# Kernel tuning notes

Hardware: AMD Instinct MI355X
Metric: run time of the kernel (lower is better)

## Reference

```python
import jax, jax.numpy as jnp
import numpy as np

N = 4096          # num_nodes
E = 65536         # num edges (avg degree 16)
WALK_LENGTH = 16
OUT_DIM = 8


def setup_inputs() -> dict:
    key = jax.random.key(0)
    k1, k2 = jax.random.split(key, 2)
    edge_index = jax.random.randint(k1, (2, E), 0, N, dtype=jnp.int64)
    # nn.Linear(walk_length, out_dim): weight [out_dim, walk_length], bias [out_dim]
    linear_w = (jax.random.normal(k2, (OUT_DIM, WALK_LENGTH), jnp.float32)
                / np.float32(np.sqrt(WALK_LENGTH)))
    linear_b = jnp.zeros((OUT_DIM,), jnp.float32)
    return {"edge_index": edge_index, "num_nodes": N,
            "linear_w": linear_w, "linear_b": linear_b}


def reference(edge_index, num_nodes, linear_w, linear_b):
    row, col = edge_index[0], edge_index[1]
    # out-degree via scatter_add, clamped to >= 1
    deg = jnp.zeros((num_nodes,), jnp.float32).at[row].add(1.0)
    deg = jnp.maximum(deg, 1.0)
    rw_values = 1.0 / deg[row]                              # [E]
    # random-walk transition matrix P[row, col] = 1/deg[row]
    # (.at[].add sums duplicate edges, matching coalesce())
    P = jnp.zeros((num_nodes, num_nodes), jnp.float32).at[row, col].add(rw_values)
    Pt = P.T

    def step(cur, _):
        cur = Pt @ cur                                      # [N, N]
        return cur, jnp.diagonal(cur)                       # k-step return probs

    cur0 = jnp.eye(num_nodes, dtype=jnp.float32)
    _, diags = jax.lax.scan(step, cur0, None, length=WALK_LENGTH)
    rw_diag = diags.T                                       # [N, walk_length]
    return rw_diag @ linear_w.T + linear_b                  # [N, out_dim]
```

## Files before the change

### kernel.cpp

```cpp
#include <hip/hip_runtime.h>
#include <hip/hip_fp16.h>
#include <hip/hip_fp8.h>

#define NNODES 4096
#define LWALK 16
#define ODIM 8

#define FP8_SCALE 256.0f
#define FP8_INV   0.00390625f
#define FP8_INV2  1.52587890625e-05f

typedef unsigned int uint4n __attribute__((ext_vector_type(4)));
typedef unsigned int uint2n __attribute__((ext_vector_type(2)));
typedef float float2n __attribute__((ext_vector_type(2)));

__device__ __forceinline__ void dec8f(unsigned int lo, unsigned int hi, float* f) {
#if __has_builtin(__builtin_amdgcn_cvt_pk_f32_fp8)
    float2n p;
    p = __builtin_amdgcn_cvt_pk_f32_fp8((int)lo, false); f[0] = p.x; f[1] = p.y;
    p = __builtin_amdgcn_cvt_pk_f32_fp8((int)lo, true);  f[2] = p.x; f[3] = p.y;
    p = __builtin_amdgcn_cvt_pk_f32_fp8((int)hi, false); f[4] = p.x; f[5] = p.y;
    p = __builtin_amdgcn_cvt_pk_f32_fp8((int)hi, true);  f[6] = p.x; f[7] = p.y;
#else
    unsigned int w[2] = {lo, hi};
    const unsigned char* b = (const unsigned char*)w;
#pragma unroll
    for (int i = 0; i < 8; ++i) {
        __hip_fp8_e4m3 t; t.__x = b[i]; f[i] = (float)t;
    }
#endif
}

__device__ __forceinline__ void enc8f(const float* a, unsigned int* lo,
                                      unsigned int* hi) {
#if __has_builtin(__builtin_amdgcn_cvt_pk_fp8_f32)
    int l = 0, h = 0;
    l = __builtin_amdgcn_cvt_pk_fp8_f32(a[0], a[1], l, false);
    l = __builtin_amdgcn_cvt_pk_fp8_f32(a[2], a[3], l, true);
    h = __builtin_amdgcn_cvt_pk_fp8_f32(a[4], a[5], h, false);
    h = __builtin_amdgcn_cvt_pk_fp8_f32(a[6], a[7], h, true);
    *lo = (unsigned int)l; *hi = (unsigned int)h;
#else
    unsigned char b[8];
#pragma unroll
    for (int i = 0; i < 8; ++i)
        b[i] = __hip_cvt_float_to_fp8(a[i], __HIP_SATFINITE, __HIP_E4M3);
    unsigned int w[2];
    __builtin_memcpy(w, b, 8);
    *lo = w[0]; *hi = w[1];
#endif
}

__device__ __forceinline__ void dec16f(uint4n w, float* f) {
    dec8f(w.x, w.y, f);
    dec8f(w.z, w.w, f + 8);
}

__device__ __forceinline__ uint4n enc16f(const float* a) {
    uint4n o;
    unsigned int lo, hi;
    enc8f(a, &lo, &hi);     o.x = lo; o.y = hi;
    enc8f(a + 8, &lo, &hi); o.z = lo; o.w = hi;
    return o;
}

__global__ void detect_fmt_k(const void* ei, int E, int* flag) {
    if (blockIdx.x == 0 && threadIdx.x == 0) {
        const long long* p = (const long long*)ei;
        int ok = 1;
        for (int i = 0; i < 64; ++i) {
            long long v = p[i];
            if (v < 0 || v >= NNODES) { ok = 0; break; }
        }
        *flag = ok;
    }
}

__device__ __forceinline__ int load_idx(const void* p, int i, int fmt) {
    if (fmt) return (int)((const long long*)p)[i];
    return ((const int*)p)[i];
}

__global__ void build_deg_cnt_k(const void* ei, int E, int* deg, int* cnt,
                                const int* fmt) {
    int e = blockIdx.x * blockDim.x + threadIdx.x;
    if (e >= E) return;
    int f = *fmt;
    int r = load_idx(ei, e, f);
    int c = load_idx(ei, E + e, f);
    atomicAdd(&deg[r], 1);
    atomicAdd(&cnt[c], 1);
}

__global__ void scan_k(const int* __restrict__ cnt, int* __restrict__ rowptr,
                       int* __restrict__ cursor) {
    __shared__ int sm[1024];
    int tid = threadIdx.x;
    int v0 = (cnt[4 * tid + 0] + 7) & ~7;
    int v1 = (cnt[4 * tid + 1] + 7) & ~7;
    int v2 = (cnt[4 * tid + 2] + 7) & ~7;
    int v3 = (cnt[4 * tid + 3] + 7) & ~7;
    int tsum = v0 + v1 + v2 + v3;
    sm[tid] = tsum;
    __syncthreads();
    int val = tsum;
    for (int off = 1; off < 1024; off <<= 1) {
        int t = (tid >= off) ? sm[tid - off] : 0;
        __syncthreads();
        val += t;
        sm[tid] = val;
        __syncthreads();
    }
    int excl = val - tsum;
    int p0 = excl, p1 = excl + v0, p2 = p1 + v1, p3 = p2 + v2;
    rowptr[4 * tid + 0] = p0; rowptr[4 * tid + 1] = p1;
    rowptr[4 * tid + 2] = p2; rowptr[4 * tid + 3] = p3;
    cursor[4 * tid + 0] = p0; cursor[4 * tid + 1] = p1;
    cursor[4 * tid + 2] = p2; cursor[4 * tid + 3] = p3;
    if (tid == 1023) rowptr[4096] = val;
}

__global__ void fill_csr_k(const void* ei, int E, const int* __restrict__ deg,
                           int* cursor, uint2* __restrict__ epad, const int* fmt) {
    int e = blockIdx.x * blockDim.x + threadIdx.x;
    if (e >= E) return;
    int f = *fmt;
    int r = load_idx(ei, e, f);
    int c = load_idx(ei, E + e, f);
    int pos = atomicAdd(&cursor[c], 1);
    int d = deg[r];
    float v = 1.0f / (float)(d < 1 ? 1 : d);
    epad[pos] = make_uint2((unsigned)r, __float_as_uint(v));
}

__global__ void pad_fill_k(const int* __restrict__ rowptr,
                           const int* __restrict__ cursor,
                           uint2* __restrict__ epad) {
    int c = blockIdx.x * blockDim.x + threadIdx.x;
    if (c >= NNODES) return;
    for (int p = cursor[c]; p < rowptr[c + 1]; ++p)
        epad[p] = make_uint2(0u, 0u);
}

__global__ __launch_bounds__(256) void x2build_k(
    const int* __restrict__ rowptr, const uint2* __restrict__ epad,
    unsigned char* __restrict__ Y8, float* __restrict__ rw) {
    __shared__ float row[NNODES];
    __shared__ float dia1;
    const int c = blockIdx.x;
    const int t = threadIdx.x;
    for (int i = t; i < NNODES; i += 256) row[i] = 0.f;
    if (t == 0) dia1 = 0.f;
    __syncthreads();
    const int beg = rowptr[c], end = rowptr[c + 1];
    for (int i1 = beg + t; i1 < end; i1 += 256) {
        uint2 e1 = epad[i1];
        float v = __uint_as_float(e1.y);
        if (v != 0.f) {
            int r = (int)e1.x;
            if (r == c) atomicAdd(&dia1, v);
            int b2 = rowptr[r], n2 = rowptr[r + 1];
            for (int j = b2; j < n2; ++j) {
                uint2 e2 = epad[j];
                float w = __uint_as_float(e2.y);
                if (w != 0.f) atomicAdd(&row[e2.x], v * w);
            }
        }
    }
    __syncthreads();
    if (t == 0) {
        rw[c * LWALK + 0] = dia1;
        rw[c * LWALK + 1] = row[c];
    }
    float f[16];
    const int base = t * 16;
#pragma unroll
    for (int u = 0; u < 16; ++u) f[u] = row[base + u] * FP8_SCALE;
    uint4n o = enc16f(f);
    __builtin_nontemporal_store(o, (uint4n*)(Y8 + (size_t)c * NNODES + base));
}

__global__ __launch_bounds__(256) void fused8_k(
    const unsigned char* __restrict__ X8, unsigned char* __restrict__ Y8,
    const int* __restrict__ rowptr, const uint2* __restrict__ epad,
    float* __restrict__ rw, int kcol,
    const unsigned char* __restrict__ PA, const unsigned char* __restrict__ PB,
    int colO, int colE, int nspmm) {
    __shared__ __half bt[64][66];
    __shared__ __half ct[64][66];
    const int bid = blockIdx.x;
    if (bid < nspmm) {
        const int slab = bid & 3;
        const int lane = threadIdx.x & 63;
        const int c =
            __builtin_amdgcn_readfirstlane((bid >> 2) * 4 + (threadIdx.x >> 6));
        const int colo = slab * 1024 + lane * 16;
        const unsigned char* Xs = X8 + colo;
        const int beg = rowptr[c], end = rowptr[c + 1];
        float a[16];
#pragma unroll
        for (int u = 0; u < 16; ++u) a[u] = 0.f;
        for (int e = beg; e < end; e += 8) {
            uint2 ed[8];
#pragma unroll
            for (int j = 0; j < 8; ++j) ed[j] = epad[e + j];
            uint4n x[8];
#pragma unroll
            for (int j = 0; j < 8; ++j)
                x[j] = *(const uint4n*)(Xs + (size_t)ed[j].x * NNODES);
#pragma unroll
            for (int j = 0; j < 8; ++j) {
                float v = __uint_as_float(ed[j].y);
                float f[16];
                dec16f(x[j], f);
#pragma unroll
                for (int u = 0; u < 16; ++u) a[u] = fmaf(f[u], v, a[u]);
            }
        }
        if ((c >> 10) == slab && lane == ((c & 1023) >> 4)) {
            float d = 0.f;
#pragma unroll
            for (int u = 0; u < 16; ++u)
                if ((c & 15) == u) d = a[u];
            rw[c * LWALK + kcol] = d * FP8_INV;
        }
        uint4n o = enc16f(a);
        __builtin_nontemporal_store(o, (uint4n*)(Y8 + (size_t)c * NNODES + colo));
    } else {
        const int pb = bid - nspmm;
        const int i0 = (pb & 63) * 64;
        const int Jbeg = (pb >> 6) * (NNODES / 16);
        const int Jend = Jbeg + (NNODES / 16);
        const int t = threadIdx.x;
        const int li = t >> 2;
        const int q = t & 3;
        const int c0 = q * 16;
        float accO = 0.f, accE = 0.f;
        for (int J = Jbeg; J < Jend; J += 64) {
            uint4n b16 = __builtin_nontemporal_load(
                (const uint4n*)(PB + (size_t)(J + li) * NNODES + i0 + c0));
            uint4n g16 = __builtin_nontemporal_load(
                (const uint4n*)(PA + (size_t)(J + li) * NNODES + i0 + c0));
            __syncthreads();
            float bf[16], gf[16];
            dec16f(b16, bf);
            dec16f(g16, gf);
#pragma unroll
            for (int s = 0; s < 16; ++s) {
                bt[c0 + s][li] = __float2half(bf[s]);
                ct[c0 + s][li] = __float2half(gf[s]);
            }
            __syncthreads();
            uint4n a16 = __builtin_nontemporal_load(
                (const uint4n*)(PA + (size_t)(i0 + li) * NNODES + J + c0));
            float af[16];
            dec16f(a16, af);
#pragma unroll
            for (int s = 0; s < 16; ++s) {
                accO = fmaf(af[s], __half2float(bt[li][c0 + s]), accO);
                accE = fmaf(af[s], __half2float(ct[li][c0 + s]), accE);
            }
        }
        accO += __shfl_xor(accO, 1);
        accO += __shfl_xor(accO, 2);
        accE += __shfl_xor(accE, 1);
        accE += __shfl_xor(accE, 2);
        if (q == 0) {
            atomicAdd(&rw[(i0 + li) * LWALK + colO], accO * FP8_INV2);
            atomicAdd(&rw[(i0 + li) * LWALK + colE], accE * FP8_INV2);
        }
    }
}

__global__ void linear_k(const float* __restrict__ rw, const float* __restrict__ W,
                         const float* __restrict__ b, float* __restrict__ out) {
    int i = blockIdx.x * blockDim.x + threadIdx.x;
    if (i >= NNODES * ODIM) return;
    int s = i >> 3, d = i & 7;
    float acc = b[d];
#pragma unroll
    for (int k = 0; k < LWALK; ++k)
        acc = fmaf(rw[s * LWALK + k], W[d * LWALK + k], acc);
    out[i] = acc;
}

extern "C" void kernel_launch(void* const* d_in, const int* in_sizes, int n_in,
                              void* d_out, int out_size, void* d_ws, size_t ws_size,
                              hipStream_t stream) {
    const void* ei = d_in[0];
    int E = in_sizes[0] / 2;
    const float* W = (const float*)d_in[2];
    const float* bias = (const float*)d_in[3];
    float* out = (float*)d_out;

    char* ws = (char*)d_ws;
    size_t off = 0;
    auto alloc = [&](size_t bytes) -> char* {
        char* p = ws + off;
        off = (off + bytes + 255) & ~(size_t)255;
        return p;
    };
    int* flag = (int*)alloc(4);
    int* deg = (int*)alloc(NNODES * 4);
    int* cnt = (int*)alloc(NNODES * 4);
    int* rowptr = (int*)alloc((NNODES + 1) * 4);
    int* cursor = (int*)alloc(NNODES * 4);
    uint2* epad = (uint2*)alloc(((size_t)E + 8 * NNODES) * 8);
    float* rw = (float*)alloc(NNODES * LWALK * 4);
    unsigned char* A = (unsigned char*)alloc((size_t)NNODES * NNODES);
    unsigned char* B = (unsigned char*)alloc((size_t)NNODES * NNODES);
    unsigned char* C = (unsigned char*)alloc((size_t)NNODES * NNODES);

    (void)hipMemsetAsync(deg, 0, NNODES * 4, stream);
    (void)hipMemsetAsync(cnt, 0, NNODES * 4, stream);
    (void)hipMemsetAsync(rw, 0, NNODES * LWALK * 4, stream);
    detect_fmt_k<<<1, 64, 0, stream>>>(ei, E, flag);
    build_deg_cnt_k<<<(E + 255) / 256, 256, 0, stream>>>(ei, E, deg, cnt, flag);
    scan_k<<<1, 1024, 0, stream>>>(cnt, rowptr, cursor);
    fill_csr_k<<<(E + 255) / 256, 256, 0, stream>>>(ei, E, deg, cursor, epad, flag);
    pad_fill_k<<<(NNODES + 255) / 256, 256, 0, stream>>>(rowptr, cursor, epad);

    x2build_k<<<NNODES, 256, 0, stream>>>(rowptr, epad, A, rw);

    const int SG = 4096;
    fused8_k<<<SG, 256, 0, stream>>>(A, B, rowptr, epad, rw, 2, nullptr, nullptr, 0, 0, SG);
    fused8_k<<<SG, 256, 0, stream>>>(B, C, rowptr, epad, rw, 3, nullptr, nullptr, 0, 0, SG);
    fused8_k<<<SG, 256, 0, stream>>>(C, A, rowptr, epad, rw, 4, nullptr, nullptr, 0, 0, SG);
    fused8_k<<<SG + 1024, 256, 0, stream>>>(A, B, rowptr, epad, rw, 5, A, C, 8, 9, SG);
    fused8_k<<<SG + 1024, 256, 0, stream>>>(B, C, rowptr, epad, rw, 6, B, A, 10, 11, SG);
    fused8_k<<<SG + 1024, 256, 0, stream>>>(C, A, rowptr, epad, rw, 7, C, B, 12, 13, SG);
    fused8_k<<<1024, 256, 0, stream>>>(nullptr, nullptr, rowptr, epad, rw, 0, A, C, 14, 15, 0);

    linear_k<<<(NNODES * ODIM + 255) / 256, 256, 0, stream>>>(rw, W, bias, out);
}
```

Before: 304.8 us.

## Pack FP8 math, pad rows to 4, split x2build inner loop, fp32 shared tiles

Several changes land together. Row padding drops from 8 to 4 with a 4-wide edge unroll in the SpMM, so fewer padded zero edges are processed. x2build now splits each neighbor's row across 16 lanes, so each two-hop expansion no longer runs serially on one thread. FP8 decode and accumulation use packed float2 vector math, the pair-product tiles move to fp32 shared memory, and the final pair pass gets its own kernel. The fp32 tiles double LDS use, which may lower occupancy.

Result: slower. 326.6 us (+7.2%).

```diff
diff --git a/kernel.cpp b/kernel.cpp
--- a/kernel.cpp
+++ b/kernel.cpp
@@ -14,21 +14,27 @@
 typedef unsigned int uint2n __attribute__((ext_vector_type(2)));
 typedef float float2n __attribute__((ext_vector_type(2)));
 
+__device__ __forceinline__ void dec4x2(unsigned int w, float2n* lo, float2n* hi) {
+#if __has_builtin(__builtin_amdgcn_cvt_pk_f32_fp8)
+    *lo = __builtin_amdgcn_cvt_pk_f32_fp8((int)w, false);
+    *hi = __builtin_amdgcn_cvt_pk_f32_fp8((int)w, true);
+#else
+    const unsigned char* b = (const unsigned char*)&w;
+    __hip_fp8_e4m3 t0, t1, t2, t3;
+    t0.__x = b[0]; t1.__x = b[1]; t2.__x = b[2]; t3.__x = b[3];
+    float2n l, h;
+    l.x = (float)t0; l.y = (float)t1;
+    h.x = (float)t2; h.y = (float)t3;
+    *lo = l; *hi = h;
+#endif
+}
+
 __device__ __forceinline__ void dec8f(unsigned int lo, unsigned int hi, float* f) {
-#if __has_builtin(__builtin_amdgcn_cvt_pk_f32_fp8)
-    float2n p;
-    p = __builtin_amdgcn_cvt_pk_f32_fp8((int)lo, false); f[0] = p.x; f[1] = p.y;
-    p = __builtin_amdgcn_cvt_pk_f32_fp8((int)lo, true);  f[2] = p.x; f[3] = p.y;
-    p = __builtin_amdgcn_cvt_pk_f32_fp8((int)hi, false); f[4] = p.x; f[5] = p.y;
-    p = __builtin_amdgcn_cvt_pk_f32_fp8((int)hi, true);  f[6] = p.x; f[7] = p.y;
-#else
-    unsigned int w[2] = {lo, hi};
-    const unsigned char* b = (const unsigned char*)w;
-#pragma unroll
-    for (int i = 0; i < 8; ++i) {
-        __hip_fp8_e4m3 t; t.__x = b[i]; f[i] = (float)t;
-    }
-#endif
+    float2n a, b, c, d;
+    dec4x2(lo, &a, &b);
+    dec4x2(hi, &c, &d);
+    f[0] = a.x; f[1] = a.y; f[2] = b.x; f[3] = b.y;
+    f[4] = c.x; f[5] = c.y; f[6] = d.x; f[7] = d.y;
 }
 
 __device__ __forceinline__ void enc8f(const float* a, unsigned int* lo,
@@ -56,14 +62,6 @@
     dec8f(w.z, w.w, f + 8);
 }
 
-__device__ __forceinline__ uint4n enc16f(const float* a) {
-    uint4n o;
-    unsigned int lo, hi;
-    enc8f(a, &lo, &hi);     o.x = lo; o.y = hi;
-    enc8f(a + 8, &lo, &hi); o.z = lo; o.w = hi;
-    return o;
-}
-
 __global__ void detect_fmt_k(const void* ei, int E, int* flag) {
     if (blockIdx.x == 0 && threadIdx.x == 0) {
         const long long* p = (const long long*)ei;
@@ -96,10 +94,10 @@
                        int* __restrict__ cursor) {
     __shared__ int sm[1024];
     int tid = threadIdx.x;
-    int v0 = (cnt[4 * tid + 0] + 7) & ~7;
-    int v1 = (cnt[4 * tid + 1] + 7) & ~7;
-    int v2 = (cnt[4 * tid + 2] + 7) & ~7;
-    int v3 = (cnt[4 * tid + 3] + 7) & ~7;
+    int v0 = (cnt[4 * tid + 0] + 3) & ~3;
+    int v1 = (cnt[4 * tid + 1] + 3) & ~3;
+    int v2 = (cnt[4 * tid + 2] + 3) & ~3;
+    int v3 = (cnt[4 * tid + 3] + 3) & ~3;
     int tsum = v0 + v1 + v2 + v3;
     sm[tid] = tsum;
     __syncthreads();
@@ -153,14 +151,16 @@
     if (t == 0) dia1 = 0.f;
     __syncthreads();
     const int beg = rowptr[c], end = rowptr[c + 1];
-    for (int i1 = beg + t; i1 < end; i1 += 256) {
+    const int g = t >> 4;
+    const int l = t & 15;
+    for (int i1 = beg + g; i1 < end; i1 += 16) {
         uint2 e1 = epad[i1];
         float v = __uint_as_float(e1.y);
         if (v != 0.f) {
             int r = (int)e1.x;
-            if (r == c) atomicAdd(&dia1, v);
+            if (r == c && l == 0) atomicAdd(&dia1, v);
             int b2 = rowptr[r], n2 = rowptr[r + 1];
-            for (int j = b2; j < n2; ++j) {
+            for (int j = b2 + l; j < n2; j += 16) {
                 uint2 e2 = epad[j];
                 float w = __uint_as_float(e2.y);
                 if (w != 0.f) atomicAdd(&row[e2.x], v * w);
@@ -176,8 +176,64 @@
     const int base = t * 16;
 #pragma unroll
     for (int u = 0; u < 16; ++u) f[u] = row[base + u] * FP8_SCALE;
-    uint4n o = enc16f(f);
+    uint4n o;
+    unsigned int lo, hi;
+    enc8f(f, &lo, &hi);     o.x = lo; o.y = hi;
+    enc8f(f + 8, &lo, &hi); o.z = lo; o.w = hi;
     __builtin_nontemporal_store(o, (uint4n*)(Y8 + (size_t)c * NNODES + base));
+}
+
+__device__ __forceinline__ void pair_body(
+    const unsigned char* __restrict__ PA, const unsigned char* __restrict__ PB,
+    float* __restrict__ rw, int colO, int colE, int pb,
+    float (*bt)[66], float (*ct)[66]) {
+    const int i0 = (pb & 63) * 64;
+    const int Jbeg = (pb >> 6) * (NNODES / 16);
+    const int Jend = Jbeg + (NNODES / 16);
+    const int t = threadIdx.x;
+    const int li = t >> 2;
+    const int q = t & 3;
+    const int c0 = q * 16;
+    float2n accO2 = {0.f, 0.f}, accE2 = {0.f, 0.f};
+    for (int J = Jbeg; J < Jend; J += 64) {
+        uint4n b16 = __builtin_nontemporal_load(
+            (const uint4n*)(PB + (size_t)(J + li) * NNODES + i0 + c0));
+        uint4n g16 = __builtin_nontemporal_load(
+            (const uint4n*)(PA + (size_t)(J + li) * NNODES + i0 + c0));
+        __syncthreads();
+        float bf[16], gf[16];
+        dec16f(b16, bf);
+        dec16f(g16, gf);
+#pragma unroll
+        for (int s = 0; s < 16; ++s) {
+            bt[c0 + s][li] = bf[s];
+            ct[c0 + s][li] = gf[s];
+        }
+        __syncthreads();
+        uint4n a16 = __builtin_nontemporal_load(
+            (const uint4n*)(PA + (size_t)(i0 + li) * NNODES + J + c0));
+        float2n af2[8];
+#pragma unroll
+        for (int u = 0; u < 4; ++u)
+            dec4x2(a16[u], &af2[2 * u], &af2[2 * u + 1]);
+        const float2n* brow = (const float2n*)&bt[li][c0];
+        const float2n* crow = (const float2n*)&ct[li][c0];
+#pragma unroll
+        for (int s = 0; s < 8; ++s) {
+            accO2 = af2[s] * brow[s] + accO2;
+            accE2 = af2[s] * crow[s] + accE2;
+        }
+    }
+    float accO = accO2.x + accO2.y;
+    float accE = accE2.x + accE2.y;
+    accO += __shfl_xor(accO, 1);
+    accO += __shfl_xor(accO, 2);
+    accE += __shfl_xor(accE, 1);
+    accE += __shfl_xor(accE, 2);
+    if (q == 0) {
+        atomicAdd(&rw[(i0 + li) * LWALK + colO], accO * FP8_INV2);
+        atomicAdd(&rw[(i0 + li) * LWALK + colE], accE * FP8_INV2);
+    }
 }
 
 __global__ __launch_bounds__(256) void fused8_k(
@@ -186,8 +242,8 @@
     float* __restrict__ rw, int kcol,
     const unsigned char* __restrict__ PA, const unsigned char* __restrict__ PB,
     int colO, int colE, int nspmm) {
-    __shared__ __half bt[64][66];
-    __shared__ __half ct[64][66];
+    __shared__ float bt[64][66];
+    __shared__ float ct[64][66];
     const int bid = blockIdx.x;
     if (bid < nspmm) {
         const int slab = bid & 3;
@@ -197,79 +253,63 @@
         const int colo = slab * 1024 + lane * 16;
         const unsigned char* Xs = X8 + colo;
         const int beg = rowptr[c], end = rowptr[c + 1];
-        float a[16];
-#pragma unroll
-        for (int u = 0; u < 16; ++u) a[u] = 0.f;
-        for (int e = beg; e < end; e += 8) {
-            uint2 ed[8];
-#pragma unroll
-            for (int j = 0; j < 8; ++j) ed[j] = epad[e + j];
-            uint4n x[8];
-#pragma unroll
-            for (int j = 0; j < 8; ++j)
+        float2n a2[8];
+#pragma unroll
+        for (int u = 0; u < 8; ++u) a2[u] = (float2n){0.f, 0.f};
+        for (int e = beg; e < end; e += 4) {
+            uint2 ed[4];
+#pragma unroll
+            for (int j = 0; j < 4; ++j) ed[j] = epad[e + j];
+            uint4n x[4];
+#pragma unroll
+            for (int j = 0; j < 4; ++j)
                 x[j] = *(const uint4n*)(Xs + (size_t)ed[j].x * NNODES);
 #pragma unroll
-            for (int j = 0; j < 8; ++j) {
+            for (int j = 0; j < 4; ++j) {
                 float v = __uint_as_float(ed[j].y);
-                float f[16];
-                dec16f(x[j], f);
-#pragma unroll
-                for (int u = 0; u < 16; ++u) a[u] = fmaf(f[u], v, a[u]);
+                float2n v2 = {v, v};
+#pragma unroll
+                for (int u = 0; u < 4; ++u) {
+                    float2n p0, p1;
+                    dec4x2(x[j][u], &p0, &p1);
+                    a2[2 * u]     = p0 * v2 + a2[2 * u];
+                    a2[2 * u + 1] = p1 * v2 + a2[2 * u + 1];
+                }
             }
         }
         if ((c >> 10) == slab && lane == ((c & 1023) >> 4)) {
+            const int dsel = c & 15;
             float d = 0.f;
 #pragma unroll
-            for (int u = 0; u < 16; ++u)
-                if ((c & 15) == u) d = a[u];
+            for (int u = 0; u < 8; ++u)
+                if ((dsel >> 1) == u) {
+                    float2n tv = a2[u];
+                    d = (dsel & 1) ? tv.y : tv.x;
+                }
             rw[c * LWALK + kcol] = d * FP8_INV;
         }
-        uint4n o = enc16f(a);
+        float f[16];
+#pragma unroll
+        for (int u = 0; u < 8; ++u) {
+            f[2 * u] = a2[u].x;
+            f[2 * u + 1] = a2[u].y;
+        }
+        uint4n o;
+        unsigned int lo, hi;
+        enc8f(f, &lo, &hi);     o.x = lo; o.y = hi;
+        enc8f(f + 8, &lo, &hi); o.z = lo; o.w = hi;
         __builtin_nontemporal_store(o, (uint4n*)(Y8 + (size_t)c * NNODES + colo));
     } else {
-        const int pb = bid - nspmm;
-        const int i0 = (pb & 63) * 64;
-        const int Jbeg = (pb >> 6) * (NNODES / 16);
-        const int Jend = Jbeg + (NNODES / 16);
-        const int t = threadIdx.x;
-        const int li = t >> 2;
-        const int q = t & 3;
-        const int c0 = q * 16;
-        float accO = 0.f, accE = 0.f;
-        for (int J = Jbeg; J < Jend; J += 64) {
-            uint4n b16 = __builtin_nontemporal_load(
-                (const uint4n*)(PB + (size_t)(J + li) * NNODES + i0 + c0));
-            uint4n g16 = __builtin_nontemporal_load(
-                (const uint4n*)(PA + (size_t)(J + li) * NNODES + i0 + c0));
-            __syncthreads();
-            float bf[16], gf[16];
-            dec16f(b16, bf);
-            dec16f(g16, gf);
-#pragma unroll
-            for (int s = 0; s < 16; ++s) {
-                bt[c0 + s][li] = __float2half(bf[s]);
-                ct[c0 + s][li] = __float2half(gf[s]);
-            }
-            __syncthreads();
-            uint4n a16 = __builtin_nontemporal_load(
-                (const uint4n*)(PA + (size_t)(i0 + li) * NNODES + J + c0));
-            float af[16];
-            dec16f(a16, af);
-#pragma unroll
-            for (int s = 0; s < 16; ++s) {
-                accO = fmaf(af[s], __half2float(bt[li][c0 + s]), accO);
-                accE = fmaf(af[s], __half2float(ct[li][c0 + s]), accE);
-            }
-        }
-        accO += __shfl_xor(accO, 1);
-        accO += __shfl_xor(accO, 2);
-        accE += __shfl_xor(accE, 1);
-        accE += __shfl_xor(accE, 2);
-        if (q == 0) {
-            atomicAdd(&rw[(i0 + li) * LWALK + colO], accO * FP8_INV2);
-            atomicAdd(&rw[(i0 + li) * LWALK + colE], accE * FP8_INV2);
-        }
-    }
+        pair_body(PA, PB, rw, colO, colE, bid - nspmm, bt, ct);
+    }
+}
+
+__global__ __launch_bounds__(256) void finale_k(
+    const unsigned char* __restrict__ PA, const unsigned char* __restrict__ PB,
+    float* __restrict__ rw) {
+    __shared__ float bt[64][66];
+    __shared__ float ct[64][66];
+    pair_body(PA, PB, rw, 14, 15, blockIdx.x, bt, ct);
 }
 
 __global__ void linear_k(const float* __restrict__ rw, const float* __restrict__ W,
@@ -305,7 +345,7 @@
     int* cnt = (int*)alloc(NNODES * 4);
     int* rowptr = (int*)alloc((NNODES + 1) * 4);
     int* cursor = (int*)alloc(NNODES * 4);
-    uint2* epad = (uint2*)alloc(((size_t)E + 8 * NNODES) * 8);
+    uint2* epad = (uint2*)alloc(((size_t)E + 4 * NNODES) * 8);
     float* rw = (float*)alloc(NNODES * LWALK * 4);
     unsigned char* A = (unsigned char*)alloc((size_t)NNODES * NNODES);
     unsigned char* B = (unsigned char*)alloc((size_t)NNODES * NNODES);
@@ -329,7 +369,6 @@
     fused8_k<<<SG + 1024, 256, 0, stream>>>(A, B, rowptr, epad, rw, 5, A, C, 8, 9, SG);
     fused8_k<<<SG + 1024, 256, 0, stream>>>(B, C, rowptr, epad, rw, 6, B, A, 10, 11, SG);
     fused8_k<<<SG + 1024, 256, 0, stream>>>(C, A, rowptr, epad, rw, 7, C, B, 12, 13, SG);
-    fused8_k<<<1024, 256, 0, stream>>>(nullptr, nullptr, rowptr, epad, rw, 0, A, C, 14, 15, 0);
-
+    finale_k<<<1024, 256, 0, stream>>>(A, C, rw);
     linear_k<<<(NNODES * ODIM + 255) / 256, 256, 0, stream>>>(rw, W, bias, out);
 }
```
